# Optimization experiments

Measured on AMD Instinct MI355X. Metric: run time of the kernel, lower is better.

Reference implementation:

```python
import jax, jax.numpy as jnp
import numpy as np

V, D, H, L = 6000, 512, 512, 2
B, S, T = 32, 6, 32
PAD, SOS, EOS1, EOS2 = 0, 1, 2, 3
EPS = 1e-5


def layer_norm(x, g, b):
    m = x.mean(-1, keepdims=True)
    v = ((x - m) ** 2).mean(-1, keepdims=True)
    return (x - m) / jnp.sqrt(v + EPS) * g + b


def lstm_stack_step(x, h, c, Wih_list, Whh, bias):
    # x: [B, in], h/c: [L, B, H]; pytorch gate order i,f,g,o
    hs, cs = [], []
    inp = x
    for l in range(L):
        gates = inp @ Wih_list[l].T + h[l] @ Whh[l].T + bias[l]
        i, f, g, o = jnp.split(gates, 4, axis=-1)
        c2 = jax.nn.sigmoid(f) * c[l] + jax.nn.sigmoid(i) * jnp.tanh(g)
        h2 = jax.nn.sigmoid(o) * jnp.tanh(c2)
        hs.append(h2); cs.append(c2); inp = h2
    return jnp.stack(hs), jnp.stack(cs)


def run_encoder(tokens, h, c, enc_emb, enc_Wih, enc_Whh, enc_b, ln_g, ln_b):
    emb = enc_emb[tokens]  # [B,T,D]
    def step(carry, x_t):
        hh, cc = lstm_stack_step(x_t, carry[0], carry[1], [enc_Wih[0], enc_Wih[1]], enc_Whh, enc_b)
        return (hh, cc), hh[-1]
    (h, c), outs = jax.lax.scan(step, (h, c), emb.transpose(1, 0, 2))
    outs = layer_norm(outs.transpose(1, 0, 2), ln_g, ln_b)  # [B,T,H]
    return outs, h, c


def decode_sentence(dec_tokens, h, c, enc_outs, mask, dec_emb, att_W, att_b, att_v,
                    dec_Wih0, dec_Wih1, dec_Whh, dec_b, ln_g, ln_b, fc_W, fc_b):
    emb = dec_emb[dec_tokens]  # [B,T,D]
    def step(carry, x_t):
        h, c = carry
        if enc_outs is None:
            context = jnp.zeros((x_t.shape[0], H), x_t.dtype)
        else:
            q = jnp.broadcast_to(h[-1][:, None, :], enc_outs.shape)  # [B,T,H]
            e = jnp.tanh(jnp.concatenate([q, enc_outs], -1) @ att_W.T + att_b)
            scores = jnp.where(mask, -1e9, e @ att_v)  # [B,T]
            a = jax.nn.softmax(scores, axis=1)
            context = jnp.einsum('bt,bth->bh', a, enc_outs)
        x = jnp.concatenate([x_t, context], -1)
        h, c = lstm_stack_step(x, h, c, [dec_Wih0, dec_Wih1], dec_Whh, dec_b)
        return (h, c), h[-1]
    (h, c), outs = jax.lax.scan(step, (h, c), emb.transpose(1, 0, 2))
    outs = layer_norm(outs, ln_g, ln_b)  # [T,B,H]
    logits = outs @ fc_W.T + fc_b        # [T,B,V]
    return logits.transpose(1, 0, 2), h, c


def setup_inputs() -> dict:
    key = jax.random.key(0)
    ks = jax.random.split(key, 20)
    w = lambda k, *s: jax.random.normal(k, s, jnp.float32) * 0.02
    enc_emb = w(ks[0], V, D).at[PAD].set(0.0)
    dec_emb = w(ks[1], V, D).at[PAD].set(0.0)
    return {
        'inputs': jax.random.randint(ks[2], (B, S, T), 0, V),
        'targets': jax.random.randint(ks[3], (B, S - 1, T), 0, V),
        'enc_emb': enc_emb,
        'enc_Wih': w(ks[4], L, 4 * H, D),
        'enc_Whh': w(ks[5], L, 4 * H, H),
        'enc_b': jnp.zeros((L, 4 * H), jnp.float32),
        'enc_ln_g': jnp.ones((H,), jnp.float32),
        'enc_ln_b': jnp.zeros((H,), jnp.float32),
        'dec_emb': dec_emb,
        'att_W': w(ks[6], H, 2 * H),
        'att_b': jnp.zeros((H,), jnp.float32),
        'att_v': w(ks[7], H),
        'dec_Wih0': w(ks[8], 4 * H, D + H),
        'dec_Wih1': w(ks[9], 4 * H, H),
        'dec_Whh': w(ks[10], L, 4 * H, H),
        'dec_b': jnp.zeros((L, 4 * H), jnp.float32),
        'dec_ln_g': jnp.ones((H,), jnp.float32),
        'dec_ln_b': jnp.zeros((H,), jnp.float32),
        'fc_W': w(ks[11], V, H),
        'fc_b': jnp.zeros((V,), jnp.float32),
    }


def reference(inputs, targets, enc_emb, enc_Wih, enc_Whh, enc_b, enc_ln_g, enc_ln_b,
              dec_emb, att_W, att_b, att_v, dec_Wih0, dec_Wih1, dec_Whh, dec_b,
              dec_ln_g, dec_ln_b, fc_W, fc_b):
    # teacher_force_ratio = 1.0 (deterministic), dropout in eval mode
    dec_h = jnp.zeros((L, B, H), jnp.float32)
    dec_c = jnp.zeros((L, B, H), jnp.float32)
    enc_h = jnp.zeros((L, B, H), jnp.float32)
    enc_c = jnp.zeros((L, B, H), jnp.float32)
    enc_outs = None
    mask = jnp.zeros((B, T), bool)
    sent_logits = []
    for s in range(S):
        tok = inputs[:, 0, :] if s == 0 else targets[:, s - 1, :]
        dec_in = jnp.concatenate([jnp.full((B, 1), SOS, tok.dtype), tok[:, :-1]], 1)
        logits, dec_h, dec_c = decode_sentence(dec_in, dec_h, dec_c, enc_outs, mask,
                                               dec_emb, att_W, att_b, att_v,
                                               dec_Wih0, dec_Wih1, dec_Whh, dec_b,
                                               dec_ln_g, dec_ln_b, fc_W, fc_b)
        if s > 0:
            sent_logits.append(logits)
        # mask for the NEXT sentence: positions strictly after the first EOS
        is_eos = (tok == EOS1) | (tok == EOS2)
        seen = jnp.cumsum(is_eos.astype(jnp.int32), axis=1) > 0
        mask = jnp.concatenate([jnp.zeros((B, 1), bool), seen[:, :-1]], 1)
        if s < S - 1:
            enc_outs, enc_h, enc_c = run_encoder(tok, enc_h, enc_c, enc_emb, enc_Wih,
                                                 enc_Whh, enc_b, enc_ln_g, enc_ln_b)
    return jnp.stack(sent_logits, axis=1)  # [B, S-1, T, V]
```

## Files before the change

kernel.cpp:

```cpp
#include <hip/hip_runtime.h>

typedef unsigned short u16;
typedef __attribute__((ext_vector_type(8))) short bf8;
typedef __attribute__((ext_vector_type(4))) float f4;
typedef __attribute__((ext_vector_type(4))) unsigned int u32x4;

struct Params {
  const int* inputs; const int* targets;
  const void *enc_emb, *enc_Wih, *enc_Whh, *enc_bias, *enc_ln_g, *enc_ln_b;
  const void *dec_emb, *att_W, *att_b, *att_v;
  const void *dec_Wih0, *dec_Wih1, *dec_Whh, *dec_bias, *dec_ln_g, *dec_ln_b;
  const void *fc_W, *fc_b;
  void* out;
};

__device__ __align__(16) u16 gb_enc_emb[3072000];
__device__ __align__(16) u16 gb_dec_emb[3072000];
__device__ __align__(16) u16 gb_enc_Wih[2097152];
__device__ __align__(16) u16 gb_enc_Whh[2097152];
__device__ __align__(16) u16 gb_dec_Wih0[2097152];
__device__ __align__(16) u16 gb_dec_Wih1[1048576];
__device__ __align__(16) u16 gb_dec_Whh[2097152];
__device__ __align__(16) u16 gb_att_W[524288];
__device__ __align__(16) u16 gb_fc_W[3072000];
__device__ float gc_enc_bias[4096], gc_dec_bias[4096];
__device__ float gc_enc_ln_g[512], gc_enc_ln_b[512], gc_dec_ln_g[512], gc_dec_ln_b[512];
__device__ float gc_att_b[512], gc_att_v[512], gc_fc_b[6000];

__device__ __align__(16) u16 g_Hdec[4 * 32 * 512];
__device__ __align__(16) u16 g_Henc[4 * 32 * 512];
__device__ __align__(16) u16 g_ctx[32 * 512];
__device__ __align__(16) u16 g_outsb5[5 * 1024 * 512];
__device__ __align__(16) u16 g_lnouts5[5 * 1024 * 512];
__device__ __align__(16) u16 g_encraw5[5 * 1024 * 512];
__device__ __align__(16) u16 g_encouts5[5 * 1024 * 512];
__device__ __align__(16) u16 g_encpart5[5 * 1024 * 512];
__device__ __align__(16) float g_pqp[32 * 512 * 32];
__device__ int g_masks[6 * 32 * 32];
__device__ int g_dtoks[6 * 32 * 32];
__device__ int g_etoks[5 * 32 * 32];

__device__ __align__(16) float g_dpre[192 * 2048 * 32];
__device__ __align__(16) float g_epre[160 * 2048 * 32];

__device__ unsigned g_flags_enc[64 * 32], g_acks_enc[64 * 32];
__device__ unsigned g_flags_dec[64 * 32], g_acks_dec[64 * 32];
__device__ unsigned g_gen0_enc, g_gen0_dec, g_encdone, g_epoch;

#define GL_OFF   0
#define HL_OFF   8704
#define CL_OFF   10752
#define SEG1_OFF 12800
#define SEG2_OFF 78336
#define LDS_TOTAL 143872

#define SPIN_CAP (1 << 27)

__device__ __forceinline__ float b2f(u16 u) { union { unsigned i; float f; } v; v.i = ((unsigned)u) << 16; return v.f; }
__device__ __forceinline__ u16 f2b(float f) {
  union { float f; unsigned i; } v; v.f = f;
  unsigned x = v.i;
  return (u16)((x + 0x7fffu + ((x >> 16) & 1u)) >> 16);
}
__device__ __forceinline__ float sigf(float x) { return 1.f / (1.f + __expf(-x)); }
__device__ __forceinline__ float tanhf_(float x) { float e = __expf(2.f * x); return 1.f - 2.f / (e + 1.f); }

__device__ __forceinline__ bool is_f32(const Params& P) {
  return *(const unsigned*)P.enc_ln_g == 0x3F800000u;
}

#define VWAIT(N) do { asm volatile("s_waitcnt vmcnt(" #N ")" ::: "memory"); \
                      __builtin_amdgcn_sched_barrier(0); } while (0)

__device__ __forceinline__ void sc_ld(bf8& d, const u16* p) {
  asm volatile("global_load_dwordx4 %0, %1, off sc0 sc1" : "=v"(d) : "v"(p));
}
__device__ __forceinline__ void sc_ld_f4(f4& d, const float* p) {
  asm volatile("global_load_dwordx4 %0, %1, off sc0 sc1" : "=v"(d) : "v"(p));
}
__device__ __forceinline__ void sc_st16(u16* p, u32x4 v) {
  asm volatile("global_store_dwordx4 %0, %1, off sc0 sc1" :: "v"(p), "v"(v) : "memory");
}
__device__ __forceinline__ void sc_st_u16(u16* p, u16 v) {
  unsigned vv = v;
  asm volatile("global_store_short %0, %1, off sc0 sc1" :: "v"(p), "v"(vv) : "memory");
}
__device__ __forceinline__ void sc_st_f32(float* p, float v) {
  asm volatile("global_store_dword %0, %1, off sc0 sc1" :: "v"(p), "v"(v) : "memory");
}
__device__ __forceinline__ unsigned sc_ld_u32(const unsigned* p) {
  unsigned r;
  asm volatile("global_load_dword %0, %1, off sc0 sc1\n\ts_waitcnt vmcnt(0)"
               : "=v"(r) : "v"(p) : "memory");
  return r;
}
__device__ __forceinline__ void sc_st_u32(unsigned* p, unsigned v) {
  asm volatile("global_store_dword %0, %1, off sc0 sc1\n\ts_waitcnt vmcnt(0)"
               :: "v"(p), "v"(v) : "memory");
}

__device__ __forceinline__ void bar_dom(unsigned* flags, unsigned* acks, int lb, int tid, unsigned& g) {
  g += 1;
  asm volatile("s_waitcnt vmcnt(0)" ::: "memory");
  __syncthreads();
  if (lb == 0) {
    if (tid >= 1 && tid < 64) {
      int it = 0;
      while (sc_ld_u32(flags + tid * 32) != g && ++it < SPIN_CAP) __builtin_amdgcn_s_sleep(2);
      sc_st_u32(acks + tid * 32, g);
    }
    __syncthreads();
  } else {
    if (tid == 0) {
      sc_st_u32(flags + lb * 32, g);
      int it = 0;
      while (sc_ld_u32(acks + lb * 32) != g && ++it < SPIN_CAP) __builtin_amdgcn_s_sleep(2);
    }
    __syncthreads();
  }
}

struct Acc2 { f4 lo, hi; };

__device__ __forceinline__ void mm_seg(Acc2& a, const u16* A, const u16* Wp, int ldW, int K, int lane) {
  const int n = lane & 15, q = lane >> 4;
  const u16* a0 = A + n * 512 + q * 8;
  const u16* a1 = a0 + 16 * 512;
  const u16* bp = Wp + n * ldW + q * 8;
  for (int k = 0; k < K; k += 32) {
    bf8 va0 = *(const bf8*)(a0 + k);
    bf8 va1 = *(const bf8*)(a1 + k);
    bf8 vb  = *(const bf8*)(bp + k);
    a.lo = __builtin_amdgcn_mfma_f32_16x16x32_bf16(va0, vb, a.lo, 0, 0, 0);
    a.hi = __builtin_amdgcn_mfma_f32_16x16x32_bf16(va1, vb, a.hi, 0, 0, 0);
  }
}

__device__ __forceinline__ void mm_tok(Acc2& a, const u16* emb, const int* toks,
                                       const u16* Wp, int ldW, int lane) {
  const int n = lane & 15, q = lane >> 4;
  const u16* a0 = emb + (size_t)toks[n] * 512 + q * 8;
  const u16* a1 = emb + (size_t)toks[n + 16] * 512 + q * 8;
  const u16* bp = Wp + n * ldW + q * 8;
  for (int k = 0; k < 512; k += 32) {
    bf8 va0 = *(const bf8*)(a0 + k);
    bf8 va1 = *(const bf8*)(a1 + k);
    bf8 vb  = *(const bf8*)(bp + k);
    a.lo = __builtin_amdgcn_mfma_f32_16x16x32_bf16(va0, vb, a.lo, 0, 0, 0);
    a.hi = __builtin_amdgcn_mfma_f32_16x16x32_bf16(va1, vb, a.hi, 0, 0, 0);
  }
}

__device__ __forceinline__ void mm_seg_llc(Acc2& a, const u16* A, const u16* Wl, int lane) {
  const int n = lane & 15, q = lane >> 4, x = n & 7;
  const u16* a0 = A + n * 512 + q * 8;
  const u16* a1 = a0 + 8192;
  const u16* wr = Wl + n * 512;
  bf8 r0[2][4], r1[2][4];
#pragma unroll
  for (int j = 0; j < 4; j++) { sc_ld(r0[0][j], a0 + j * 32); sc_ld(r1[0][j], a1 + j * 32); }
#pragma unroll
  for (int c = 0; c < 4; c++) {
    const int pb = c & 1, nb = pb ^ 1;
    if (c < 3) {
#pragma unroll
      for (int j = 0; j < 4; j++) {
        sc_ld(r0[nb][j], a0 + (c + 1) * 128 + j * 32);
        sc_ld(r1[nb][j], a1 + (c + 1) * 128 + j * 32);
      }
      VWAIT(8);
    } else {
      VWAIT(0);
    }
#pragma unroll
    for (int j = 0; j < 4; j++) {
      int ki = c * 4 + j;
      bf8 vb = *(const bf8*)(wr + (((q + 4 * ki) ^ x) << 3));
      a.lo = __builtin_amdgcn_mfma_f32_16x16x32_bf16(r0[pb][j], vb, a.lo, 0, 0, 0);
      a.hi = __builtin_amdgcn_mfma_f32_16x16x32_bf16(r1[pb][j], vb, a.hi, 0, 0, 0);
    }
  }
}

__device__ __forceinline__ void stage_seg(u16* lds_seg, const u16* W, int ldW, int c0, int u, int tid) {
  for (int idx = tid; idx < 4096; idx += 256) {
    int w = idx >> 10, n = (idx >> 6) & 15, ch = idx & 63;
    const u16* src = W + (size_t)(w * 512 + u * 16 + n) * ldW + c0 + ch * 8;
    u16* dst = lds_seg + ((w * 16 + n) * 64 + (ch ^ (n & 7))) * 8;
    *(u32x4*)dst = *(const u32x4*)src;
  }
}

__device__ __forceinline__ void lstm_llc(char* smem, int u, int lane, int wave, int tid,
    const float* pre, const float* bias,
    const u16* A1, const u16* A2,
    u16* Hout, u16* Xtra, int xmode, int t, bool do_pqp)
{
  float* gl = (float*)(smem + GL_OFF);
  float* hl = (float*)(smem + HL_OFF);
  float* Cl = (float*)(smem + CL_OFF);
  const u16* seg1 = (const u16*)(smem + SEG1_OFF) + wave * 8192;
  const u16* seg2 = (const u16*)(smem + SEG2_OFF) + wave * 8192;
  const int n = lane & 15, q = lane >> 4;
  const int colbase = wave * 512 + u * 16;
  Acc2 acc;
  if (pre) {
    const float* pb = pre + (size_t)(colbase + n) * 32;
    acc.lo = *(const f4*)(pb + q * 4);
    acc.hi = *(const f4*)(pb + q * 4 + 16);
  } else {
    float bv = bias[colbase + n];
    f4 bi = { bv, bv, bv, bv };
    acc.lo = bi; acc.hi = bi;
  }
  if (A1) mm_seg_llc(acc, A1, seg1, lane);
  if (A2) mm_seg_llc(acc, A2, seg2, lane);
#pragma unroll
  for (int r = 0; r < 4; r++) {
    gl[(wave * 32 + q * 4 + r) * 17 + n]      = acc.lo[r];
    gl[(wave * 32 + 16 + q * 4 + r) * 17 + n] = acc.hi[r];
  }
  __syncthreads();
  for (int p = tid; p < 512; p += 256) {
    int b = p >> 4, nn = p & 15, hc = u * 16 + nn;
    float iv = gl[(0 * 32 + b) * 17 + nn];
    float fv = gl[(1 * 32 + b) * 17 + nn];
    float gv = gl[(2 * 32 + b) * 17 + nn];
    float ov = gl[(3 * 32 + b) * 17 + nn];
    float c2 = sigf(fv) * Cl[b * 16 + nn] + sigf(iv) * tanhf_(gv);
    float h2 = sigf(ov) * tanhf_(c2);
    Cl[b * 16 + nn] = c2;
    u16 hb = f2b(h2);
    sc_st_u16(Hout + b * 512 + hc, hb);
    if (xmode == 1)      Xtra[(t * 32 + b) * 512 + hc] = hb;
    else if (xmode == 2) sc_st_u16(Xtra + (b * 32 + t) * 512 + hc, hb);
    if (do_pqp) hl[b * 16 + nn] = h2;
  }
  if (do_pqp) {
    __syncthreads();
    for (int h = tid; h < 512; h += 256) {
      float wl[16];
#pragma unroll
      for (int j = 0; j < 16; j++) wl[j] = b2f(gb_att_W[h * 1024 + u * 16 + j]);
      for (int b = 0; b < 32; b++) {
        float sacc = 0.f;
#pragma unroll
        for (int j = 0; j < 16; j++) sacc += hl[b * 16 + j] * wl[j];
        sc_st_f32(g_pqp + ((size_t)b * 512 + h) * 32 + u, sacc);
      }
    }
  }
}

__device__ __forceinline__ void att_llc(char* smem, int b, int s, int lane, int wave, int tid)
{
  float* qp = (float*)(smem + GL_OFF); float* sc = qp + 512; float* av = sc + 32;
  const u16* ep_prev = g_encpart5 + (size_t)(s - 1) * 524288;
  const u16* eo_prev = g_encouts5 + (size_t)(s - 1) * 524288;

  for (int h = tid; h < 512; h += 256) {
    const float* pp = g_pqp + ((size_t)b * 512 + h) * 32;
    f4 r[8];
#pragma unroll
    for (int j = 0; j < 8; j++) sc_ld_f4(r[j], pp + j * 4);
    VWAIT(0);
    f4 ss = r[0];
#pragma unroll
    for (int j = 1; j < 8; j++) ss += r[j];
    qp[h] = ss[0] + ss[1] + ss[2] + ss[3];
  }
  __syncthreads();
  for (int tt = wave; tt < 32; tt += 4) {
    float part = 0.f;
    for (int h = lane; h < 512; h += 64)
      part += tanhf_(qp[h] + b2f(ep_prev[(b * 32 + tt) * 512 + h])) * gc_att_v[h];
#pragma unroll
    for (int off = 32; off; off >>= 1) part += __shfl_xor(part, off, 64);
    if (lane == 0) sc[tt] = g_masks[(s * 32 + b) * 32 + tt] ? -1e9f : fminf(fmaxf(part, -1e30f), 1e30f);
  }
  __syncthreads();
  if (wave == 0) {
    float v = (lane < 32) ? sc[lane] : -3e38f;
    float m = v;
#pragma unroll
    for (int off = 32; off; off >>= 1) m = fmaxf(m, __shfl_xor(m, off, 64));
    float e = (lane < 32) ? __expf(v - m) : 0.f;
    float ssum = e;
#pragma unroll
    for (int off = 32; off; off >>= 1) ssum += __shfl_xor(ssum, off, 64);
    if (lane < 32) av[lane] = e / ssum;
  }
  __syncthreads();
  for (int h = tid; h < 512; h += 256) {
    float ssum = 0.f;
#pragma unroll 4
    for (int tt = 0; tt < 32; tt++) ssum += av[tt] * b2f(eo_prev[(b * 32 + tt) * 512 + h]);
    sc_st_u16(g_ctx + b * 512 + h, f2b(ssum));
  }
}


__global__ void __launch_bounds__(256) k_conv(Params P)
{
  const bool f32 = is_f32(P);
  int c = blockIdx.x * 256 + threadIdx.x;
  const void* src; u16* dst;
  if (c < 384000)                 { src = P.enc_emb;  dst = gb_enc_emb;  }
  else if ((c -= 384000) < 384000){ src = P.dec_emb;  dst = gb_dec_emb;  }
  else if ((c -= 384000) < 262144){ src = P.enc_Wih;  dst = gb_enc_Wih;  }
  else if ((c -= 262144) < 262144){ src = P.enc_Whh;  dst = gb_enc_Whh;  }
  else if ((c -= 262144) < 262144){ src = P.dec_Wih0; dst = gb_dec_Wih0; }
  else if ((c -= 262144) < 131072){ src = P.dec_Wih1; dst = gb_dec_Wih1; }
  else if ((c -= 131072) < 262144){ src = P.dec_Whh;  dst = gb_dec_Whh;  }
  else if ((c -= 262144) < 65536) { src = P.att_W;    dst = gb_att_W;    }
  else                            { c -= 65536; src = P.fc_W; dst = gb_fc_W; }
  if (f32) {
    const float* s = (const float*)src + (size_t)c * 8;
    union { u32x4 v; u16 o[8]; } u;
#pragma unroll
    for (int j = 0; j < 8; j++) u.o[j] = f2b(s[j]);
    *(u32x4*)(dst + (size_t)c * 8) = u.v;
  } else {
    ((u32x4*)dst)[c] = ((const u32x4*)src)[c];
  }
}

__global__ void __launch_bounds__(256) k_conv_small(Params P)
{
  const bool f32 = is_f32(P);
  int i = blockIdx.x * 256 + threadIdx.x;
  const void* src; float* dst;
  if (i < 4096)                 { src = P.enc_bias; dst = gc_enc_bias; }
  else if ((i -= 4096) < 4096)  { src = P.dec_bias; dst = gc_dec_bias; }
  else if ((i -= 4096) < 512)   { src = P.enc_ln_g; dst = gc_enc_ln_g; }
  else if ((i -= 512) < 512)    { src = P.enc_ln_b; dst = gc_enc_ln_b; }
  else if ((i -= 512) < 512)    { src = P.dec_ln_g; dst = gc_dec_ln_g; }
  else if ((i -= 512) < 512)    { src = P.dec_ln_b; dst = gc_dec_ln_b; }
  else if ((i -= 512) < 512)    { src = P.att_b;    dst = gc_att_b;    }
  else if ((i -= 512) < 512)    { src = P.att_v;    dst = gc_att_v;    }
  else if ((i -= 512) < 6000)   { src = P.fc_b;     dst = gc_fc_b;     }
  else return;
  dst[i] = f32 ? ((const float*)src)[i] : b2f(((const u16*)src)[i]);
}

__global__ void __launch_bounds__(256) k_setup(Params P)
{
  const int gtid = blockIdx.x * 256 + threadIdx.x;
  if (gtid == 0) g_epoch = g_epoch + 1;
  if (gtid < 6144) {
    int s = gtid >> 10, rem = gtid & 1023, t = rem >> 5, b = rem & 31;
    int tok = (t == 0) ? 1
            : ((s == 0) ? P.inputs[b * 192 + (t - 1)] : P.targets[b * 160 + (s - 1) * 32 + (t - 1)]);
    g_dtoks[gtid] = tok;
  } else if (gtid < 6144 + 5120) {
    int gi = gtid - 6144;
    int s = gi >> 10, rem = gi & 1023, t = rem >> 5, b = rem & 31;
    g_etoks[gi] = (s == 0) ? P.inputs[b * 192 + t] : P.targets[b * 160 + (s - 1) * 32 + t];
  }
  if (blockIdx.x >= 64 && blockIdx.x < 224 && threadIdx.x == 0) {
    int w = blockIdx.x - 64;
    int s = 1 + (w >> 5), b = w & 31;
    int seen = 0;
    g_masks[(s * 32 + b) * 32 + 0] = 0;
    for (int t2 = 1; t2 < 32; t2++) {
      int tk = (s == 1) ? P.inputs[b * 192 + (t2 - 1)] : P.targets[b * 160 + (s - 2) * 32 + (t2 - 1)];
      seen |= (tk == 2 || tk == 3) ? 1 : 0;
      g_masks[(s * 32 + b) * 32 + t2] = seen;
    }
  }
  u32x4 z = { 0u, 0u, 0u, 0u };
  if (gtid < 8192)  ((u32x4*)g_Hdec)[gtid] = z;
  if (gtid >= 8192 && gtid < 16384) ((u32x4*)g_Henc)[gtid - 8192] = z;
  if (gtid >= 16384 && gtid < 18432) ((u32x4*)g_ctx)[gtid - 16384] = z;
}

__global__ void __launch_bounds__(256) k_pre()
{
  const int blk = blockIdx.x, tid = threadIdx.x;
  const int lane = tid & 63, wave = tid >> 6;
  const int n = lane & 15, q = lane >> 4;
  const bool dec = blk < 1536;
  const int idx = dec ? blk : blk - 1536;
  const int u = idx & 31, gq = idx >> 5;
  const u16* emb = dec ? gb_dec_emb : gb_enc_emb;
  const u16* W   = dec ? gb_dec_Wih0 : gb_enc_Wih;
  const int ldW  = dec ? 1024 : 512;
  const float* bias = dec ? gc_dec_bias : gc_enc_bias;
  float* pre = dec ? g_dpre : g_epre;
  const int* toks = dec ? g_dtoks : g_etoks;
  const int colbase = wave * 512 + u * 16;
  for (int gi = 0; gi < 4; gi++) {
    int gstep = gq * 4 + gi;
    float bv = bias[colbase + n];
    f4 bi = { bv, bv, bv, bv };
    Acc2 acc; acc.lo = bi; acc.hi = bi;
    mm_tok(acc, emb, toks + gstep * 32, W + (size_t)colbase * ldW, ldW, lane);
    float* dst = pre + ((size_t)gstep * 2048 + colbase + n) * 32;
    *(f4*)(dst + q * 4) = acc.lo;
    *(f4*)(dst + q * 4 + 16) = acc.hi;
  }
}

__global__ void __launch_bounds__(256) k_persist()
{
  extern __shared__ char smem[];
  const int blk = blockIdx.x, tid = threadIdx.x;
  const int lane = tid & 63, wave = tid >> 6;
  const bool encdom = blk < 64;
  const int lb = encdom ? blk : blk - 64;
  const int role = lb >> 5, u = lb & 31;
  const unsigned epoch = g_epoch;

  { float* Cl = (float*)(smem + CL_OFF); for (int i = tid; i < 512; i += 256) Cl[i] = 0.f; }

  u16* s1 = (u16*)(smem + SEG1_OFF);
  u16* s2 = (u16*)(smem + SEG2_OFF);
  if (encdom) {
    if (role == 0) {
      stage_seg(s1, gb_enc_Whh, 512, 0, u, tid);
    } else {
      stage_seg(s1, gb_enc_Wih + 1048576, 512, 0, u, tid);
      stage_seg(s2, gb_enc_Whh + 1048576, 512, 0, u, tid);
    }
  } else {
    if (role == 0) {
      stage_seg(s1, gb_dec_Wih0, 1024, 512, u, tid);
      stage_seg(s2, gb_dec_Whh, 512, 0, u, tid);
    } else {
      stage_seg(s1, gb_dec_Wih1, 512, 0, u, tid);
      stage_seg(s2, gb_dec_Whh + 1048576, 512, 0, u, tid);
    }
  }
  __syncthreads();

  unsigned* flags = encdom ? g_flags_enc : g_flags_dec;
  unsigned* acks  = encdom ? g_acks_enc  : g_acks_dec;
  unsigned g = sc_ld_u32(encdom ? &g_gen0_enc : &g_gen0_dec);

  if (encdom) {
    for (int s = 0; s < 5; s++) {
      for (int t = 0; t < 32; t++) {
        const int gstep = s * 32 + t, si = gstep & 1, so = si ^ 1;
        if (role == 0)
          lstm_llc(smem, u, lane, wave, tid,
            g_epre + (size_t)gstep * 65536, nullptr,
            g_Henc + (si * 2 + 0) * 16384, nullptr,
            g_Henc + (so * 2 + 0) * 16384, nullptr, 0, t, false);
        bar_dom(flags, acks, lb, tid, g);
        if (role == 1)
          lstm_llc(smem, u, lane, wave, tid,
            nullptr, gc_enc_bias + 2048,
            g_Henc + (so * 2 + 0) * 16384, g_Henc + (si * 2 + 1) * 16384,
            g_Henc + (so * 2 + 1) * 16384, g_encraw5 + (size_t)s * 524288, 2, t, false);
        bar_dom(flags, acks, lb, tid, g);
      }
      {
        const u16* in = g_encraw5 + (size_t)s * 524288;
        u16* out = g_encouts5 + (size_t)s * 524288;
#pragma unroll
        for (int rr = 0; rr < 4; rr++) {
          int row = lb * 16 + wave * 4 + rr;
          const u16* x = in + row * 512 + lane * 8;
          float xs[8]; float sm = 0.f, sq = 0.f;
#pragma unroll
          for (int j = 0; j < 8; j++) { xs[j] = b2f(x[j]); sm += xs[j]; sq += xs[j] * xs[j]; }
#pragma unroll
          for (int off = 32; off; off >>= 1) { sm += __shfl_xor(sm, off, 64); sq += __shfl_xor(sq, off, 64); }
          float mean = sm * (1.f / 512.f);
          float var = fmaxf(sq * (1.f / 512.f) - mean * mean, 0.f);
          float rstd = rsqrtf(var + 1e-5f);
          union { u32x4 v; u16 o[8]; } pk;
#pragma unroll
          for (int j = 0; j < 8; j++) {
            int k = lane * 8 + j;
            pk.o[j] = f2b((xs[j] - mean) * rstd * gc_enc_ln_g[k] + gc_enc_ln_b[k]);
          }
          sc_st16(out + row * 512 + lane * 8, pk.v);
        }
      }
      bar_dom(flags, acks, lb, tid, g);
      {
        const u16* eo = g_encouts5 + (size_t)s * 524288;
        u16* ep = g_encpart5 + (size_t)s * 524288;
        const int n = lane & 15, q = lane >> 4;
        int rc = lb >> 3, cc = lb & 7;
        int nbase = cc * 64 + wave * 16;
        float bv = gc_att_b[nbase + n];
#pragma unroll
        for (int mt = 0; mt < 4; mt++) {
          int rowbase = rc * 128 + mt * 32;
          f4 bi = { bv, bv, bv, bv };
          Acc2 acc; acc.lo = bi; acc.hi = bi;
          mm_seg(acc, eo + rowbase * 512, gb_att_W + nbase * 1024 + 512, 1024, 512, lane);
#pragma unroll
          for (int r = 0; r < 4; r++) {
            int row = rowbase + q * 4 + r;
            sc_st_u16(ep + row * 512 + nbase + n, f2b(acc.lo[r]));
            sc_st_u16(ep + (row + 16) * 512 + nbase + n, f2b(acc.hi[r]));
          }
        }
      }
      bar_dom(flags, acks, lb, tid, g);
      if (lb == 0 && tid == 0) sc_st_u32(&g_encdone, epoch * 8u + (unsigned)s + 1u);
    }
    if (lb == 0 && tid == 0) sc_st_u32(&g_gen0_enc, g);
  } else {
    for (int s = 0; s < 6; s++) {
      if (s >= 1) {
        if (tid == 0) {
          unsigned tgt = epoch * 8u + (unsigned)s;
          int it = 0;
          while ((int)(sc_ld_u32(&g_encdone) - tgt) < 0 && ++it < SPIN_CAP)
            __builtin_amdgcn_s_sleep(8);
        }
        __syncthreads();
      }
      for (int t = 0; t < 32; t++) {
        const int gstep = s * 32 + t, si = gstep & 1, so = si ^ 1;
        if (role == 0 && s > 0) att_llc(smem, u, s, lane, wave, tid);
        bar_dom(flags, acks, lb, tid, g);
        if (role == 0)
          lstm_llc(smem, u, lane, wave, tid,
            g_dpre + (size_t)gstep * 65536, nullptr,
            (s > 0) ? g_ctx : nullptr, g_Hdec + (si * 2 + 0) * 16384,
            g_Hdec + (so * 2 + 0) * 16384, nullptr, 0, t, false);
        bar_dom(flags, acks, lb, tid, g);
        if (role == 1) {
          int dp = ((s > 0 && t < 31) || (t == 31 && s < 5)) ? 1 : 0;
          u16* outp = (s >= 1) ? (g_outsb5 + (size_t)(s - 1) * 524288) : nullptr;
          lstm_llc(smem, u, lane, wave, tid,
            nullptr, gc_dec_bias + 2048,
            g_Hdec + (so * 2 + 0) * 16384, g_Hdec + (si * 2 + 1) * 16384,
            g_Hdec + (so * 2 + 1) * 16384, outp, outp ? 1 : 0, t, dp != 0);
        }
        bar_dom(flags, acks, lb, tid, g);
      }
    }
    if (lb == 0 && tid == 0) sc_st_u32(&g_gen0_dec, g);
  }
}

__global__ void __launch_bounds__(256) k_ln_post(Params P)
{
  const int blk = blockIdx.x, tid = threadIdx.x;
  const int lane = tid & 63, wave = tid >> 6;
#pragma unroll
  for (int rr = 0; rr < 2; rr++) {
    int row = blk * 8 + wave * 2 + rr;
    const u16* x = g_outsb5 + (size_t)row * 512 + lane * 8;
    float xs[8]; float sm = 0.f, sq = 0.f;
#pragma unroll
    for (int j = 0; j < 8; j++) { xs[j] = b2f(x[j]); sm += xs[j]; sq += xs[j] * xs[j]; }
#pragma unroll
    for (int off = 32; off; off >>= 1) { sm += __shfl_xor(sm, off, 64); sq += __shfl_xor(sq, off, 64); }
    float mean = sm * (1.f / 512.f);
    float var = fmaxf(sq * (1.f / 512.f) - mean * mean, 0.f);
    float rstd = rsqrtf(var + 1e-5f);
    u16* o = g_lnouts5 + (size_t)row * 512 + lane * 8;
#pragma unroll
    for (int j = 0; j < 8; j++) {
      int k = lane * 8 + j;
      o[j] = f2b((xs[j] - mean) * rstd * gc_dec_ln_g[k] + gc_dec_ln_b[k]);
    }
  }
}

__global__ void __launch_bounds__(256) k_fc_post(Params P)
{
  __shared__ char sbuf[65536];
  const int blk0 = blockIdx.x, tid = threadIdx.x;
  const int sidx = blk0 / 192, blk = blk0 % 192;
  const int lane = tid & 63, wave = tid >> 6;
  const int n = lane & 15, q = lane >> 4;
  const bool f32o = is_f32(P);
  const u16* lnin = g_lnouts5 + (size_t)sidx * 524288;
  u16* As = (u16*)sbuf;
  int mc = blk / 12, ncc = blk % 12;
  int mrow0 = mc * 64;
  for (int idx = tid; idx < 64 * 64; idx += 256) {
    int row = idx >> 6, ch = idx & 63;
    int phys = ch ^ (row & 7);
    *(u32x4*)(As + (row * 64 + phys) * 8) = *(const u32x4*)(lnin + (size_t)(mrow0 + row) * 512 + ch * 8);
  }
  __syncthreads();
  f4 acc[4][8];
#pragma unroll
  for (int j = 0; j < 8; j++) {
    int c = ncc * 512 + wave * 128 + j * 16 + n;
    float bv = (c < 6000) ? gc_fc_b[c] : 0.f;
    f4 bi = { bv, bv, bv, bv };
#pragma unroll
    for (int mt = 0; mt < 4; mt++) acc[mt][j] = bi;
  }
  for (int kt = 0; kt < 16; kt++) {
    bf8 a[4];
#pragma unroll
    for (int mt = 0; mt < 4; mt++) {
      int row = mt * 16 + n;
      int ch = kt * 4 + q;
      int phys = ch ^ (row & 7);
      a[mt] = *(const bf8*)(As + (row * 64 + phys) * 8);
    }
#pragma unroll
    for (int j = 0; j < 8; j++) {
      int c = ncc * 512 + wave * 128 + j * 16 + n;
      int brow = (c < 6000) ? c : 5999;
      bf8 vb = *(const bf8*)(gb_fc_W + brow * 512 + kt * 32 + q * 8);
#pragma unroll
      for (int mt = 0; mt < 4; mt++)
        acc[mt][j] = __builtin_amdgcn_mfma_f32_16x16x32_bf16(a[mt], vb, acc[mt][j], 0, 0, 0);
    }
  }
#pragma unroll
  for (int j = 0; j < 8; j++) {
    int c = ncc * 512 + wave * 128 + j * 16 + n;
    if (c < 6000) {
#pragma unroll
      for (int mt = 0; mt < 4; mt++) {
#pragma unroll
        for (int r = 0; r < 4; r++) {
          int rix = mrow0 + mt * 16 + q * 4 + r;
          int tt = rix >> 5, b = rix & 31;
          size_t oidx = (size_t)((b * 5 + sidx) * 32 + tt) * 6000 + c;
          float v = acc[mt][j][r];
          if (f32o) ((float*)P.out)[oidx] = v;
          else      ((u16*)P.out)[oidx] = f2b(v);
        }
      }
    }
  }
}

extern "C" void kernel_launch(void* const* d_in, const int* in_sizes, int n_in,
                              void* d_out, int out_size, void* d_ws, size_t ws_size,
                              hipStream_t stream) {
  Params P;
  P.inputs   = (const int*)d_in[0];
  P.targets  = (const int*)d_in[1];
  P.enc_emb  = d_in[2];
  P.enc_Wih  = d_in[3];
  P.enc_Whh  = d_in[4];
  P.enc_bias = d_in[5];
  P.enc_ln_g = d_in[6];
  P.enc_ln_b = d_in[7];
  P.dec_emb  = d_in[8];
  P.att_W    = d_in[9];
  P.att_b    = d_in[10];
  P.att_v    = d_in[11];
  P.dec_Wih0 = d_in[12];
  P.dec_Wih1 = d_in[13];
  P.dec_Whh  = d_in[14];
  P.dec_bias = d_in[15];
  P.dec_ln_g = d_in[16];
  P.dec_ln_b = d_in[17];
  P.fc_W     = d_in[18];
  P.fc_b     = d_in[19];
  P.out = d_out;

  static bool attr_done = false;
  if (!attr_done) {
    hipFuncSetAttribute((const void*)k_persist,
                        hipFuncAttributeMaxDynamicSharedMemorySize, LDS_TOTAL);
    attr_done = true;
  }

  hipLaunchKernelGGL(k_conv, dim3(9364), dim3(256), 0, stream, P);
  hipLaunchKernelGGL(k_conv_small, dim3(68), dim3(256), 0, stream, P);
  hipLaunchKernelGGL(k_setup, dim3(256), dim3(256), 0, stream, P);
  hipLaunchKernelGGL(k_pre, dim3(2816), dim3(256), 0, stream);
  hipLaunchKernelGGL(k_persist, dim3(128), dim3(256), LDS_TOTAL, stream);
  hipLaunchKernelGGL(k_ln_post, dim3(640), dim3(256), 0, stream, P);
  hipLaunchKernelGGL(k_fc_post, dim3(960), dim3(256), 0, stream, P);
}
```

Baseline: 12.56 ms.

## Compute attention query projection locally in att_llc instead of via partial-sum buffer

```diff
diff --git a/kernel.cpp b/kernel.cpp
--- a/kernel.cpp
+++ b/kernel.cpp
@@ -35,7 +35,6 @@
 __device__ __align__(16) u16 g_encraw5[5 * 1024 * 512];
 __device__ __align__(16) u16 g_encouts5[5 * 1024 * 512];
 __device__ __align__(16) u16 g_encpart5[5 * 1024 * 512];
-__device__ __align__(16) float g_pqp[32 * 512 * 32];
 __device__ int g_masks[6 * 32 * 32];
 __device__ int g_dtoks[6 * 32 * 32];
 __device__ int g_etoks[5 * 32 * 32];
@@ -75,18 +74,12 @@
 __device__ __forceinline__ void sc_ld(bf8& d, const u16* p) {
   asm volatile("global_load_dwordx4 %0, %1, off sc0 sc1" : "=v"(d) : "v"(p));
 }
-__device__ __forceinline__ void sc_ld_f4(f4& d, const float* p) {
-  asm volatile("global_load_dwordx4 %0, %1, off sc0 sc1" : "=v"(d) : "v"(p));
-}
 __device__ __forceinline__ void sc_st16(u16* p, u32x4 v) {
   asm volatile("global_store_dwordx4 %0, %1, off sc0 sc1" :: "v"(p), "v"(v) : "memory");
 }
 __device__ __forceinline__ void sc_st_u16(u16* p, u16 v) {
   unsigned vv = v;
   asm volatile("global_store_short %0, %1, off sc0 sc1" :: "v"(p), "v"(vv) : "memory");
-}
-__device__ __forceinline__ void sc_st_f32(float* p, float v) {
-  asm volatile("global_store_dword %0, %1, off sc0 sc1" :: "v"(p), "v"(v) : "memory");
 }
 __device__ __forceinline__ unsigned sc_ld_u32(const unsigned* p) {
   unsigned r;
@@ -156,28 +149,23 @@
   const u16* a0 = A + n * 512 + q * 8;
   const u16* a1 = a0 + 8192;
   const u16* wr = Wl + n * 512;
-  bf8 r0[2][4], r1[2][4];
-#pragma unroll
-  for (int j = 0; j < 4; j++) { sc_ld(r0[0][j], a0 + j * 32); sc_ld(r1[0][j], a1 + j * 32); }
+  bf8 r0[4][4], r1[4][4];
+#pragma unroll
+  for (int c = 0; c < 4; c++)
+#pragma unroll
+    for (int j = 0; j < 4; j++) {
+      sc_ld(r0[c][j], a0 + c * 128 + j * 32);
+      sc_ld(r1[c][j], a1 + c * 128 + j * 32);
+    }
 #pragma unroll
   for (int c = 0; c < 4; c++) {
-    const int pb = c & 1, nb = pb ^ 1;
-    if (c < 3) {
-#pragma unroll
-      for (int j = 0; j < 4; j++) {
-        sc_ld(r0[nb][j], a0 + (c + 1) * 128 + j * 32);
-        sc_ld(r1[nb][j], a1 + (c + 1) * 128 + j * 32);
-      }
-      VWAIT(8);
-    } else {
-      VWAIT(0);
-    }
+    if (c == 0) VWAIT(24); else if (c == 1) VWAIT(16); else if (c == 2) VWAIT(8); else VWAIT(0);
 #pragma unroll
     for (int j = 0; j < 4; j++) {
       int ki = c * 4 + j;
       bf8 vb = *(const bf8*)(wr + (((q + 4 * ki) ^ x) << 3));
-      a.lo = __builtin_amdgcn_mfma_f32_16x16x32_bf16(r0[pb][j], vb, a.lo, 0, 0, 0);
-      a.hi = __builtin_amdgcn_mfma_f32_16x16x32_bf16(r1[pb][j], vb, a.hi, 0, 0, 0);
+      a.lo = __builtin_amdgcn_mfma_f32_16x16x32_bf16(r0[c][j], vb, a.lo, 0, 0, 0);
+      a.hi = __builtin_amdgcn_mfma_f32_16x16x32_bf16(r1[c][j], vb, a.hi, 0, 0, 0);
     }
   }
 }
@@ -194,10 +182,9 @@
 __device__ __forceinline__ void lstm_llc(char* smem, int u, int lane, int wave, int tid,
     const float* pre, const float* bias,
     const u16* A1, const u16* A2,
-    u16* Hout, u16* Xtra, int xmode, int t, bool do_pqp)
+    u16* Hout, u16* Xtra, int xmode, int t)
 {
   float* gl = (float*)(smem + GL_OFF);
-  float* hl = (float*)(smem + HL_OFF);
   float* Cl = (float*)(smem + CL_OFF);
   const u16* seg1 = (const u16*)(smem + SEG1_OFF) + wave * 8192;
   const u16* seg2 = (const u16*)(smem + SEG2_OFF) + wave * 8192;
@@ -234,40 +221,36 @@
     sc_st_u16(Hout + b * 512 + hc, hb);
     if (xmode == 1)      Xtra[(t * 32 + b) * 512 + hc] = hb;
     else if (xmode == 2) sc_st_u16(Xtra + (b * 32 + t) * 512 + hc, hb);
-    if (do_pqp) hl[b * 16 + nn] = h2;
-  }
-  if (do_pqp) {
-    __syncthreads();
-    for (int h = tid; h < 512; h += 256) {
-      float wl[16];
-#pragma unroll
-      for (int j = 0; j < 16; j++) wl[j] = b2f(gb_att_W[h * 1024 + u * 16 + j]);
-      for (int b = 0; b < 32; b++) {
-        float sacc = 0.f;
-#pragma unroll
-        for (int j = 0; j < 16; j++) sacc += hl[b * 16 + j] * wl[j];
-        sc_st_f32(g_pqp + ((size_t)b * 512 + h) * 32 + u, sacc);
-      }
-    }
-  }
-}
-
-__device__ __forceinline__ void att_llc(char* smem, int b, int s, int lane, int wave, int tid)
-{
-  float* qp = (float*)(smem + GL_OFF); float* sc = qp + 512; float* av = sc + 32;
+  }
+}
+
+__device__ __forceinline__ void att_llc(char* smem, int b, int s, int si, int lane, int wave, int tid)
+{
+  float* qp  = (float*)(smem + GL_OFF);
+  float* sc  = qp + 512;
+  float* av  = sc + 32;
+  float* hlf = av + 32;
   const u16* ep_prev = g_encpart5 + (size_t)(s - 1) * 524288;
   const u16* eo_prev = g_encouts5 + (size_t)(s - 1) * 524288;
-
+  const u16* h1 = g_Hdec + (si * 2 + 1) * 16384 + b * 512;
+
+  if (wave == 0) {
+    bf8 v; sc_ld(v, h1 + lane * 8);
+    VWAIT(0);
+#pragma unroll
+    for (int j = 0; j < 8; j++) hlf[lane * 8 + j] = b2f((u16)v[j]);
+  }
+  __syncthreads();
   for (int h = tid; h < 512; h += 256) {
-    const float* pp = g_pqp + ((size_t)b * 512 + h) * 32;
-    f4 r[8];
-#pragma unroll
-    for (int j = 0; j < 8; j++) sc_ld_f4(r[j], pp + j * 4);
-    VWAIT(0);
-    f4 ss = r[0];
-#pragma unroll
-    for (int j = 1; j < 8; j++) ss += r[j];
-    qp[h] = ss[0] + ss[1] + ss[2] + ss[3];
+    const u16* wrow = gb_att_W + (size_t)h * 1024;
+    float acc = 0.f;
+#pragma unroll 8
+    for (int kk = 0; kk < 64; kk++) {
+      bf8 w = *(const bf8*)(wrow + kk * 8);
+#pragma unroll
+      for (int j = 0; j < 8; j++) acc += hlf[kk * 8 + j] * b2f((u16)w[j]);
+    }
+    qp[h] = acc;
   }
   __syncthreads();
   for (int tt = wave; tt < 32; tt += 4) {
@@ -445,13 +428,13 @@
           lstm_llc(smem, u, lane, wave, tid,
             g_epre + (size_t)gstep * 65536, nullptr,
             g_Henc + (si * 2 + 0) * 16384, nullptr,
-            g_Henc + (so * 2 + 0) * 16384, nullptr, 0, t, false);
+            g_Henc + (so * 2 + 0) * 16384, nullptr, 0, t);
         bar_dom(flags, acks, lb, tid, g);
         if (role == 1)
           lstm_llc(smem, u, lane, wave, tid,
             nullptr, gc_enc_bias + 2048,
             g_Henc + (so * 2 + 0) * 16384, g_Henc + (si * 2 + 1) * 16384,
-            g_Henc + (so * 2 + 1) * 16384, g_encraw5 + (size_t)s * 524288, 2, t, false);
+            g_Henc + (so * 2 + 1) * 16384, g_encraw5 + (size_t)s * 524288, 2, t);
         bar_dom(flags, acks, lb, tid, g);
       }
       {
@@ -517,21 +500,20 @@
       }
       for (int t = 0; t < 32; t++) {
         const int gstep = s * 32 + t, si = gstep & 1, so = si ^ 1;
-        if (role == 0 && s > 0) att_llc(smem, u, s, lane, wave, tid);
+        if (role == 0 && s > 0) att_llc(smem, u, s, si, lane, wave, tid);
         bar_dom(flags, acks, lb, tid, g);
         if (role == 0)
           lstm_llc(smem, u, lane, wave, tid,
             g_dpre + (size_t)gstep * 65536, nullptr,
             (s > 0) ? g_ctx : nullptr, g_Hdec + (si * 2 + 0) * 16384,
-            g_Hdec + (so * 2 + 0) * 16384, nullptr, 0, t, false);
+            g_Hdec + (so * 2 + 0) * 16384, nullptr, 0, t);
         bar_dom(flags, acks, lb, tid, g);
         if (role == 1) {
-          int dp = ((s > 0 && t < 31) || (t == 31 && s < 5)) ? 1 : 0;
           u16* outp = (s >= 1) ? (g_outsb5 + (size_t)(s - 1) * 524288) : nullptr;
           lstm_llc(smem, u, lane, wave, tid,
             nullptr, gc_dec_bias + 2048,
             g_Hdec + (so * 2 + 0) * 16384, g_Hdec + (si * 2 + 1) * 16384,
-            g_Hdec + (so * 2 + 1) * 16384, outp, outp ? 1 : 0, t, dp != 0);
+            g_Hdec + (so * 2 + 1) * 16384, outp, outp ? 1 : 0, t);
         }
         bar_dom(flags, acks, lb, tid, g);
       }
```

Measured after the change: 11.51 ms. 1.09x faster.
